# Kernel tuning notes

Hardware: AMD Instinct MI355X
Metric: run time of the kernel (lower is better)

## Reference

```python
import jax, jax.numpy as jnp
import numpy as np

C = 256
D = C // 4  # shared q/k projection dim = 64
EPS_BN = 1e-5


def _bn(x, g, b, m, v):
    # inference-style BatchNorm1d over channel dim of [B, C, N]
    inv = g / jnp.sqrt(v + EPS_BN)
    return x * inv[:, None] + (b - m * inv)[:, None]


def _sa_layer(x, xyz, qk_w, v_w, v_b, tr_w, tr_b, g, b, m, var):
    h = x + xyz                                             # [B,C,N]
    q = jnp.einsum('dc,bcn->bnd', qk_w, h)                  # [B,N,D]
    k = jnp.einsum('dc,bcn->bdn', qk_w, h)                  # [B,D,N] (shared weight)
    v = jnp.einsum('oc,bcn->bon', v_w, h) + v_b[:, None]    # [B,C,N]
    energy = jnp.einsum('bnd,bdm->bnm', q, k)               # [B,N,N]
    att = jax.nn.softmax(energy, axis=-1)
    # offset-attention L1 renorm over query dim (dim=1)
    att = att / (1e-9 + att.sum(axis=1, keepdims=True))
    x_r = jnp.einsum('bcn,bnm->bcm', v, att)                # [B,C,N]
    t = jnp.einsum('oc,bcn->bon', tr_w, x - x_r) + tr_b[:, None]
    return x + jax.nn.relu(_bn(t, g, b, m, var))


def setup_inputs() -> dict:
    key = jax.random.key(0)
    ks = jax.random.split(key, 20)
    B, N = 4, 4096
    inp = {
        'x': jax.random.normal(ks[0], (B, C, N), jnp.float32),
        'xyz': jax.random.normal(ks[1], (B, N, 3), jnp.float32),
        'pos_w': jax.random.normal(ks[2], (C, 3), jnp.float32) * 0.1,
        'pos_b': jax.random.normal(ks[3], (C,), jnp.float32) * 0.05,
        'conv1_w': jax.random.normal(ks[4], (C, C), jnp.float32) * (1.0 / np.sqrt(C)),
        'bn1_g': jax.random.uniform(ks[5], (C,), jnp.float32, 0.5, 1.5),
        'bn1_b': jax.random.normal(ks[6], (C,), jnp.float32) * 0.05,
        'bn1_m': jax.random.normal(ks[7], (C,), jnp.float32) * 0.05,
        'bn1_v': jax.random.uniform(ks[8], (C,), jnp.float32, 0.5, 1.5),
        # stacked params for 4 SA layers
        'qk_w': jax.random.normal(ks[9], (4, D, C), jnp.float32) * (1.0 / np.sqrt(C)),
        'v_w': jax.random.normal(ks[10], (4, C, C), jnp.float32) * (1.0 / np.sqrt(C)),
        'v_b': jax.random.normal(ks[11], (4, C), jnp.float32) * 0.05,
        'tr_w': jax.random.normal(ks[12], (4, C, C), jnp.float32) * (1.0 / np.sqrt(C)),
        'tr_b': jax.random.normal(ks[13], (4, C), jnp.float32) * 0.05,
        'bn_g': jax.random.uniform(ks[14], (4, C), jnp.float32, 0.5, 1.5),
        'bn_b': jax.random.normal(ks[15], (4, C), jnp.float32) * 0.05,
        'bn_m': jax.random.normal(ks[16], (4, C), jnp.float32) * 0.05,
        'bn_v': jax.random.uniform(ks[17], (4, C), jnp.float32, 0.5, 1.5),
    }
    return inp


def reference(x, xyz, pos_w, pos_b, conv1_w, bn1_g, bn1_b, bn1_m, bn1_v,
              qk_w, v_w, v_b, tr_w, tr_b, bn_g, bn_b, bn_m, bn_v):
    # xyz: [B,N,3] -> permute -> [B,3,N] -> pos conv -> [B,C,N]
    pos = jnp.einsum('oc,bnc->bon', pos_w, xyz) + pos_b[:, None]
    h = jnp.einsum('oc,bcn->bon', conv1_w, x)
    h = jax.nn.relu(_bn(h, bn1_g, bn1_b, bn1_m, bn1_v))
    outs = []
    for i in range(4):
        h = _sa_layer(h, pos, qk_w[i], v_w[i], v_b[i], tr_w[i], tr_b[i],
                      bn_g[i], bn_b[i], bn_m[i], bn_v[i])
        outs.append(h)
    return jnp.concatenate(outs, axis=1)  # [B, 4C, N]
```

## Files before the change

### kernel.cpp

```cpp
#include <hip/hip_runtime.h>

#define NB 4
#define NC 256
#define ND 64
#define NN 4096

typedef unsigned short us;
using short8v = __attribute__((ext_vector_type(8))) short;
using f32x4   = __attribute__((ext_vector_type(4))) float;

#define MFMA16 __builtin_amdgcn_mfma_f32_16x16x32_bf16

constexpr size_t SBCN = (size_t)NB * NC * NN;
constexpr size_t SBN  = (size_t)NB * NN;

__device__ inline us f2bf(float f) {
  unsigned u = __builtin_bit_cast(unsigned, f);
  u += 0x7fffu + ((u >> 16) & 1u);
  return (us)(u >> 16);
}
__device__ inline float bf2f(us s) {
  unsigned u = (unsigned)s << 16;
  return __builtin_bit_cast(float, u);
}

__global__ __launch_bounds__(256) void pos_kernel(
    const float* __restrict__ xyz, const float* __restrict__ pw,
    const float* __restrict__ pb, float* __restrict__ pos)
{
  int idx = blockIdx.x * 256 + threadIdx.x;
  int n  = idx & (NN - 1);
  int tc = idx >> 12;
  int o  = tc & (NC - 1);
  int b  = tc >> 8;
  const float* xp = xyz + ((size_t)b * NN + n) * 3;
  pos[idx] = pb[o] + pw[o*3+0]*xp[0] + pw[o*3+1]*xp[1] + pw[o*3+2]*xp[2];
}

template<int O, bool ADD_P, bool HAS_BIAS, bool HAS_BN, bool RELU,
         bool HAS_RES, bool TRIPLE, bool VSPLIT, bool HAS_OUT2>
__global__ __launch_bounds__(256) void wgemm(
    const float* __restrict__ W, const float* __restrict__ H,
    const float* __restrict__ P, const float* __restrict__ bias,
    const float* __restrict__ bng, const float* __restrict__ bnb,
    const float* __restrict__ bnm, const float* __restrict__ bnv,
    const float* __restrict__ RES, float* __restrict__ OUT,
    float* __restrict__ OUT2, float* __restrict__ OUT3,
    float* __restrict__ OUT4)
{
  __shared__ float Wt[16][64];
  __shared__ float Ht[16][64];
  const int b  = blockIdx.z;
  const int o0 = blockIdx.y * 64;
  const int n0 = blockIdx.x * 64;
  const int t  = threadIdx.x;
  const int og = t >> 4, ng = t & 15;
  const int lo = t >> 2, lc4 = (t & 3) * 4;
  const int hc = t >> 4, hn4 = (t & 15) * 4;
  float acc[4][4] = {};
  for (int c0 = 0; c0 < NC; c0 += 16) {
    float4 w4 = *(const float4*)&W[(size_t)(o0 + lo) * NC + c0 + lc4];
    float4 h4 = *(const float4*)&H[((size_t)b * NC + c0 + hc) * NN + n0 + hn4];
    if (ADD_P) {
      float4 p4 = *(const float4*)&P[((size_t)b * NC + c0 + hc) * NN + n0 + hn4];
      h4.x += p4.x; h4.y += p4.y; h4.z += p4.z; h4.w += p4.w;
    }
    Wt[lc4+0][lo] = w4.x; Wt[lc4+1][lo] = w4.y;
    Wt[lc4+2][lo] = w4.z; Wt[lc4+3][lo] = w4.w;
    *(float4*)&Ht[hc][hn4] = h4;
    __syncthreads();
    #pragma unroll
    for (int cc = 0; cc < 16; ++cc) {
      float4 wv = *(const float4*)&Wt[cc][og*4];
      float4 hv = *(const float4*)&Ht[cc][ng*4];
      float wa[4] = {wv.x, wv.y, wv.z, wv.w};
      float ha[4] = {hv.x, hv.y, hv.z, hv.w};
      #pragma unroll
      for (int i = 0; i < 4; ++i)
        #pragma unroll
        for (int j = 0; j < 4; ++j)
          acc[i][j] += wa[i] * ha[j];
    }
    __syncthreads();
  }
  float vals[4][4];
  #pragma unroll
  for (int i = 0; i < 4; ++i) {
    const int o = o0 + og * 4 + i;
    float sc = 1.0f, sh = 0.0f;
    if (HAS_BIAS) sh = bias[o];
    if (HAS_BN) {
      float inv = bng[o] * rsqrtf(bnv[o] + 1e-5f);
      sh = sh * inv + (bnb[o] - bnm[o] * inv);
      sc = inv;
    }
    #pragma unroll
    for (int j = 0; j < 4; ++j) {
      float v = acc[i][j] * sc + sh;
      if (RELU) v = fmaxf(v, 0.0f);
      vals[i][j] = v;
    }
    if (HAS_RES) {
      float4 rv = *(const float4*)&RES[((size_t)b * NC + o) * NN + n0 + ng*4];
      vals[i][0] += rv.x; vals[i][1] += rv.y;
      vals[i][2] += rv.z; vals[i][3] += rv.w;
    }
  }
  if (TRIPLE) {
    us* o1 = (us*)OUT;  us* o2 = (us*)OUT2;  us* o3 = (us*)OUT3;
    #pragma unroll
    for (int j = 0; j < 4; ++j) {
      const int n = n0 + ng * 4 + j;
      us s1[4], s2[4], s3[4];
      #pragma unroll
      for (int i = 0; i < 4; ++i) {
        float v = vals[i][j];
        us h1 = f2bf(v); float r = v - bf2f(h1);
        us h2 = f2bf(r); r -= bf2f(h2);
        us h3 = f2bf(r);
        s1[i] = h1; s2[i] = h2; s3[i] = h3;
      }
      const size_t base = ((size_t)b * NN + n) * 64 + og * 4;
      uint2 u;
      u.x = (unsigned)s1[0] | ((unsigned)s1[1] << 16);
      u.y = (unsigned)s1[2] | ((unsigned)s1[3] << 16);
      *(uint2*)&o1[base] = u;
      u.x = (unsigned)s2[0] | ((unsigned)s2[1] << 16);
      u.y = (unsigned)s2[2] | ((unsigned)s2[3] << 16);
      *(uint2*)&o2[base] = u;
      u.x = (unsigned)s3[0] | ((unsigned)s3[1] << 16);
      u.y = (unsigned)s3[2] | ((unsigned)s3[3] << 16);
      *(uint2*)&o3[base] = u;
    }
  } else if (VSPLIT) {
    us* v1p = (us*)OUT; us* v2p = (us*)OUT2;
    #pragma unroll
    for (int i = 0; i < 4; ++i) {
      const int o = o0 + og * 4 + i;
      us s1[4], s2[4];
      #pragma unroll
      for (int j = 0; j < 4; ++j) {
        float v = vals[i][j];
        us h1 = f2bf(v);
        s1[j] = h1;
        s2[j] = f2bf(v - bf2f(h1));
      }
      const size_t base = ((size_t)b * NC + o) * NN + n0 + ng * 4;
      uint2 u;
      u.x = (unsigned)s1[0] | ((unsigned)s1[1] << 16);
      u.y = (unsigned)s1[2] | ((unsigned)s1[3] << 16);
      *(uint2*)&v1p[base] = u;
      u.x = (unsigned)s2[0] | ((unsigned)s2[1] << 16);
      u.y = (unsigned)s2[2] | ((unsigned)s2[3] << 16);
      *(uint2*)&v2p[base] = u;
    }
  } else {
    #pragma unroll
    for (int i = 0; i < 4; ++i) {
      const int o = o0 + og * 4 + i;
      float4 r = {vals[i][0], vals[i][1], vals[i][2], vals[i][3]};
      *(float4*)&OUT[((size_t)b * O + o) * NN + n0 + ng*4] = r;
      if (HAS_OUT2)
        *(float4*)&OUT2[((size_t)b * 4 * NC + o) * NN + n0 + ng*4] = r;
    }
  }
}

__global__ __launch_bounds__(128, 3) void rowstats_mfma(
    const us* __restrict__ q1, const us* __restrict__ q2,
    const us* __restrict__ q3,
    float* __restrict__ Mp, float* __restrict__ Lp)
{
  __shared__ us qs[3][32][72];
  const int b = blockIdx.y;
  const int n0 = blockIdx.x * 32;
  const int mk = blockIdx.z;
  const int t = threadIdx.x;
  const int w = t >> 6, l = t & 63, lm = l & 15, g = l >> 4;
  const int nrow = n0 + w * 16;
  const us* qp[3] = {q1, q2, q3};
  short8v an[3][2];
  #pragma unroll
  for (int s = 0; s < 3; ++s) {
    const size_t ab = ((size_t)b * NN + nrow + lm) * ND + 8 * g;
    an[s][0] = *(const short8v*)(qp[s] + ab);
    an[s][1] = *(const short8v*)(qp[s] + ab + 32);
  }
  float mrun[4], lrun[4];
  #pragma unroll
  for (int r = 0; r < 4; ++r) { mrun[r] = -1e30f; lrun[r] = 0.f; }

  const int nloc0 = t >> 3, d8 = (t & 7) * 8;
  const int mbeg = mk * (NN / 2), mend = mbeg + NN / 2;
  for (int m0 = mbeg; m0 < mend; m0 += 32) {
    __syncthreads();
    #pragma unroll
    for (int i = 0; i < 6; ++i) {
      const int s = i >> 1, n = (i & 1) * 16 + nloc0;
      *(short8v*)&qs[s][n][d8] =
          *(const short8v*)(qp[s] + ((size_t)b * NN + m0 + n) * ND + d8);
    }
    __syncthreads();
    float e[2][4];
    #pragma unroll
    for (int sub = 0; sub < 2; ++sub) {
      f32x4 eA = {0.f,0.f,0.f,0.f}, eB = {0.f,0.f,0.f,0.f};
      #pragma unroll
      for (int kh = 0; kh < 2; ++kh) {
        short8v b0 = *(const short8v*)&qs[0][sub*16+lm][kh*32+8*g];
        short8v b1 = *(const short8v*)&qs[1][sub*16+lm][kh*32+8*g];
        short8v b2 = *(const short8v*)&qs[2][sub*16+lm][kh*32+8*g];
        eA = MFMA16(an[0][kh], b0, eA, 0,0,0);
        eA = MFMA16(an[0][kh], b1, eA, 0,0,0);
        eA = MFMA16(an[0][kh], b2, eA, 0,0,0);
        eB = MFMA16(an[1][kh], b0, eB, 0,0,0);
        eB = MFMA16(an[2][kh], b0, eB, 0,0,0);
        eB = MFMA16(an[1][kh], b1, eB, 0,0,0);
      }
      f32x4 ee = eA + eB;
      #pragma unroll
      for (int r = 0; r < 4; ++r) e[sub][r] = ee[r];
    }
    #pragma unroll
    for (int r = 0; r < 4; ++r) {
      float mx = fmaxf(e[0][r], e[1][r]);
      float p = __expf(e[0][r] - mx) + __expf(e[1][r] - mx);
      float d = mx - mrun[r];
      if (d > 8.f) { lrun[r] = lrun[r] * __expf(-d) + p; mrun[r] = mx; }
      else          lrun[r] += p * __expf(d);
    }
  }
  #pragma unroll
  for (int r = 0; r < 4; ++r) {
    float m = mrun[r], s = lrun[r];
    #pragma unroll
    for (int off = 1; off < 16; off <<= 1) {
      float om = __shfl_xor(m, off);
      float os = __shfl_xor(s, off);
      float nm = fmaxf(m, om);
      s = s * __expf(m - nm) + os * __expf(om - nm);
      m = nm;
    }
    if (lm == 0) {
      Mp[(size_t)mk * SBN + (size_t)b * NN + nrow + 4 * g + r] = m;
      Lp[(size_t)mk * SBN + (size_t)b * NN + nrow + 4 * g + r] = s;
    }
  }
}

__global__ __launch_bounds__(256) void statmerge(
    const float* __restrict__ Mp, const float* __restrict__ Lp,
    float* __restrict__ Mr, float* __restrict__ Lr)
{
  const int i = blockIdx.x * 256 + threadIdx.x;
  float m0 = Mp[i], m1 = Mp[SBN + i];
  float l0 = Lp[i], l1 = Lp[SBN + i];
  float M = fmaxf(m0, m1);
  float L = l0 * __expf(m0 - M) + l1 * __expf(m1 - M);
  Mr[i] = M;
  Lr[i] = 1.0f / L;
}

__global__ __launch_bounds__(256, 4) void fusedatt_mfma(
    const us* __restrict__ q1, const us* __restrict__ q2,
    const us* __restrict__ q3,
    const us* __restrict__ v1, const us* __restrict__ v2,
    const float* __restrict__ Mr, const float* __restrict__ Lr,
    float* __restrict__ xr, float* __restrict__ csb)
{
  __shared__ us qs[2][3][32][72];
  __shared__ us att1[64][40];
  __shared__ us att2[64][40];
  const int b  = blockIdx.y;
  const int m0 = blockIdx.x * 64;
  const int chalf = blockIdx.z & 1;
  const int nk    = blockIdx.z >> 1;
  const int c0 = chalf * 128;
  const int t  = threadIdx.x;
  const int w  = t >> 6, l = t & 63, lm = l & 15, g = l >> 4;
  const int mrow = w * 16 + lm;
  const int mg   = m0 + mrow;
  const us* qp[3] = {q1, q2, q3};

  short8v bm[3][2];
  #pragma unroll
  for (int s = 0; s < 3; ++s) {
    const size_t mb = ((size_t)b * NN + mg) * ND + 8 * g;
    bm[s][0] = *(const short8v*)(qp[s] + mb);
    bm[s][1] = *(const short8v*)(qp[s] + mb + 32);
  }
  const float* Mb = Mr + (size_t)b * NN;
  const float* Lb = Lr + (size_t)b * NN;
  const us* vb1 = v1 + ((size_t)b * NC + c0 + w * 32 + lm) * NN + 8 * g;
  const us* vb2 = v2 + ((size_t)b * NC + c0 + w * 32 + lm) * NN + 8 * g;

  f32x4 acc[2][4];
  const f32x4 fzero = {0.f,0.f,0.f,0.f};
  #pragma unroll
  for (int cs = 0; cs < 2; ++cs)
    #pragma unroll
    for (int mm = 0; mm < 4; ++mm) acc[cs][mm] = fzero;
  float csp = 0.f;

  const int nloc = t >> 3, d8 = (t & 7) * 8;
  const int nbeg = nk * (NN / 2), nend = nbeg + NN / 2;

  #pragma unroll
  for (int i = 0; i < 3; ++i)
    *(short8v*)&qs[0][i][nloc][d8] =
        *(const short8v*)(qp[i] + ((size_t)b * NN + nbeg + nloc) * ND + d8);
  __syncthreads();

  int cur = 0;
  for (int nt = nbeg; nt < nend; nt += 32) {
    short8v nx0, nx1, nx2;
    const bool has_next = (nt + 32) < nend;
    if (has_next) {
      const size_t nb = ((size_t)b * NN + nt + 32 + nloc) * ND + d8;
      nx0 = *(const short8v*)(qp[0] + nb);
      nx1 = *(const short8v*)(qp[1] + nb);
      nx2 = *(const short8v*)(qp[2] + nb);
    }
    #pragma unroll
    for (int sub = 0; sub < 2; ++sub) {
      f32x4 eA = fzero, eB = fzero;
      #pragma unroll
      for (int kh = 0; kh < 2; ++kh) {
        short8v a0 = *(const short8v*)&qs[cur][0][sub*16+lm][kh*32+8*g];
        short8v a1 = *(const short8v*)&qs[cur][1][sub*16+lm][kh*32+8*g];
        short8v a2 = *(const short8v*)&qs[cur][2][sub*16+lm][kh*32+8*g];
        eA = MFMA16(a0, bm[0][kh], eA, 0,0,0);
        eA = MFMA16(a0, bm[1][kh], eA, 0,0,0);
        eA = MFMA16(a0, bm[2][kh], eA, 0,0,0);
        eB = MFMA16(a1, bm[0][kh], eB, 0,0,0);
        eB = MFMA16(a2, bm[0][kh], eB, 0,0,0);
        eB = MFMA16(a1, bm[1][kh], eB, 0,0,0);
      }
      f32x4 ee = eA + eB;
      float m4[4], l4[4];
      *(float4*)m4 = *(const float4*)&Mb[nt + sub*16 + 4*g];
      *(float4*)l4 = *(const float4*)&Lb[nt + sub*16 + 4*g];
      us a1r[4], a2r[4];
      #pragma unroll
      for (int r = 0; r < 4; ++r) {
        float p = __expf(ee[r] - m4[r]) * l4[r];
        csp += p;
        us hi = f2bf(p);
        a1r[r] = hi;
        a2r[r] = f2bf(p - bf2f(hi));
      }
      uint2 u;
      u.x = (unsigned)a1r[0] | ((unsigned)a1r[1] << 16);
      u.y = (unsigned)a1r[2] | ((unsigned)a1r[3] << 16);
      *(uint2*)&att1[mrow][sub*16 + 4*g] = u;
      u.x = (unsigned)a2r[0] | ((unsigned)a2r[1] << 16);
      u.y = (unsigned)a2r[2] | ((unsigned)a2r[3] << 16);
      *(uint2*)&att2[mrow][sub*16 + 4*g] = u;
    }
    if (has_next) {
      *(short8v*)&qs[cur ^ 1][0][nloc][d8] = nx0;
      *(short8v*)&qs[cur ^ 1][1][nloc][d8] = nx1;
      *(short8v*)&qs[cur ^ 1][2][nloc][d8] = nx2;
    }
    __syncthreads();
    #pragma unroll
    for (int cs = 0; cs < 2; ++cs) {
      short8v av1 = *(const short8v*)(vb1 + (size_t)cs * 16 * NN + nt);
      short8v av2 = *(const short8v*)(vb2 + (size_t)cs * 16 * NN + nt);
      #pragma unroll
      for (int mm = 0; mm < 4; ++mm) {
        short8v batt1 = *(const short8v*)&att1[mm * 16 + lm][8 * g];
        short8v batt2 = *(const short8v*)&att2[mm * 16 + lm][8 * g];
        acc[cs][mm] = MFMA16(av1, batt1, acc[cs][mm], 0,0,0);
        acc[cs][mm] = MFMA16(av2, batt1, acc[cs][mm], 0,0,0);
        acc[cs][mm] = MFMA16(av1, batt2, acc[cs][mm], 0,0,0);
      }
    }
    __syncthreads();
    cur ^= 1;
  }

  csp += __shfl_xor(csp, 16);
  csp += __shfl_xor(csp, 32);
  if (chalf == 0 && l < 16)
    csb[(size_t)nk * SBN + (size_t)b * NN + m0 + w * 16 + l] = csp;

  float* xrp = xr + (size_t)nk * SBCN;
  #pragma unroll
  for (int cs = 0; cs < 2; ++cs) {
    #pragma unroll
    for (int mm = 0; mm < 4; ++mm) {
      #pragma unroll
      for (int r = 0; r < 4; ++r) {
        const int c = c0 + w * 32 + cs * 16 + 4 * g + r;
        const int m = m0 + mm * 16 + lm;
        xrp[((size_t)b * NC + c) * NN + m] = acc[cs][mm][r];
      }
    }
  }
}

__global__ __launch_bounds__(256) void xr_reduce(
    const float* __restrict__ xr, const float* __restrict__ csb,
    const float* __restrict__ h, float* __restrict__ dbuf)
{
  const int i4 = blockIdx.x * 256 + threadIdx.x;
  const int mq = i4 & (NN / 4 - 1);
  const int bc = i4 >> 10;
  const int b  = bc >> 8;
  const size_t off = (size_t)bc * NN + mq * 4;
  float4 a0 = *(const float4*)&xr[off];
  float4 a1 = *(const float4*)&xr[SBCN + off];
  float4 hv = *(const float4*)&h[off];
  const size_t co = (size_t)b * NN + mq * 4;
  float4 c0 = *(const float4*)&csb[co];
  float4 c1 = *(const float4*)&csb[SBN + co];
  float4 r;
  r.x = hv.x - (a0.x + a1.x) / (1e-9f + c0.x + c1.x);
  r.y = hv.y - (a0.y + a1.y) / (1e-9f + c0.y + c1.y);
  r.z = hv.z - (a0.z + a1.z) / (1e-9f + c0.z + c1.z);
  r.w = hv.w - (a0.w + a1.w) / (1e-9f + c0.w + c1.w);
  *(float4*)&dbuf[off] = r;
}

extern "C" void kernel_launch(void* const* d_in, const int* in_sizes, int n_in,
                              void* d_out, int out_size, void* d_ws, size_t ws_size,
                              hipStream_t stream) {
  const float* x      = (const float*)d_in[0];
  const float* xyz    = (const float*)d_in[1];
  const float* pos_w  = (const float*)d_in[2];
  const float* pos_b  = (const float*)d_in[3];
  const float* conv1w = (const float*)d_in[4];
  const float* bn1_g  = (const float*)d_in[5];
  const float* bn1_b  = (const float*)d_in[6];
  const float* bn1_m  = (const float*)d_in[7];
  const float* bn1_v  = (const float*)d_in[8];
  const float* qk_w   = (const float*)d_in[9];
  const float* v_w    = (const float*)d_in[10];
  const float* v_b    = (const float*)d_in[11];
  const float* tr_w   = (const float*)d_in[12];
  const float* tr_b   = (const float*)d_in[13];
  const float* bn_g   = (const float*)d_in[14];
  const float* bn_b   = (const float*)d_in[15];
  const float* bn_m   = (const float*)d_in[16];
  const float* bn_v   = (const float*)d_in[17];
  float* out = (float*)d_out;
  float* ws  = (float*)d_ws;

  const size_t BCN = SBCN;
  const size_t BDN = (size_t)NB * ND * NN;
  const size_t BN  = SBN;
  float* pos  = ws;
  float* h    = pos + BCN;
  float* xr   = h   + BCN;
  float* Mr   = xr  + 2 * BCN;
  float* Lr   = Mr  + BN;
  float* csb  = Lr  + BN;
  float* Mp   = csb + 2 * BN;
  float* Lp   = Mp  + 2 * BN;
  us* qA1 = (us*)(Lp + 2 * BN);
  us* qA2 = qA1 + BDN;
  us* qA3 = qA2 + BDN;
  us* v1  = qA3 + BDN;
  us* v2  = v1  + BCN;

  pos_kernel<<<(NB * NC * NN) / 256, 256, 0, stream>>>(xyz, pos_w, pos_b, pos);

  wgemm<256, false, false, true, true, false, false, false, false>
      <<<dim3(NN/64, NC/64, NB), 256, 0, stream>>>(
          conv1w, x, nullptr, nullptr, bn1_g, bn1_b, bn1_m, bn1_v,
          nullptr, h, nullptr, nullptr, nullptr);

  for (int li = 0; li < 4; ++li) {
    const float* qw = qk_w + (size_t)li * ND * NC;
    const float* vw = v_w  + (size_t)li * NC * NC;
    const float* vb = v_b  + (size_t)li * NC;
    const float* tw = tr_w + (size_t)li * NC * NC;
    const float* tb = tr_b + (size_t)li * NC;

    wgemm<64, true, false, false, false, false, true, false, false>
        <<<dim3(NN/64, 1, NB), 256, 0, stream>>>(
            qw, h, pos, nullptr, nullptr, nullptr, nullptr, nullptr,
            nullptr, (float*)qA1, (float*)qA2, (float*)qA3, nullptr);

    wgemm<256, true, true, false, false, false, false, true, false>
        <<<dim3(NN/64, NC/64, NB), 256, 0, stream>>>(
            vw, h, pos, vb, nullptr, nullptr, nullptr, nullptr,
            nullptr, (float*)v1, (float*)v2, nullptr, nullptr);

    rowstats_mfma<<<dim3(NN/32, NB, 2), 128, 0, stream>>>(
        qA1, qA2, qA3, Mp, Lp);
    statmerge<<<(unsigned)(BN / 256), 256, 0, stream>>>(Mp, Lp, Mr, Lr);

    fusedatt_mfma<<<dim3(NN/64, NB, 4), 256, 0, stream>>>(
        qA1, qA2, qA3, v1, v2, Mr, Lr, xr, csb);

    xr_reduce<<<(unsigned)(BCN / 1024), 256, 0, stream>>>(xr, csb, h, xr);

    wgemm<256, false, true, true, true, true, false, false, true>
        <<<dim3(NN/64, NC/64, NB), 256, 0, stream>>>(
            tw, xr, nullptr, tb, bn_g + li*NC, bn_b + li*NC,
            bn_m + li*NC, bn_v + li*NC,
            h, h, out + (size_t)li * NC * NN, nullptr, nullptr);
  }
}
```

Measured before the change: 1.605 ms.

## Enlarge wgemm output tile and make attention blocks cover all channels

The fp32 weight GEMMs now use a 128-row output tile, so each thread holds 8x4 accumulators and each loaded H tile is reused across twice as many output channels. The fused attention kernel drops the channel-half split: each block computes all 256 channels, so the softmax attention tile (exp recomputation from q) is built once instead of twice. Register pressure rises and occupancy falls (launch bounds go from 4 to 2 blocks), and the attention grid halves, which may reduce latency hiding.

Result: no change. 1.614 ms (+0.6%).

```diff
diff --git a/kernel.cpp b/kernel.cpp
--- a/kernel.cpp
+++ b/kernel.cpp
@@ -37,7 +37,7 @@
   pos[idx] = pb[o] + pw[o*3+0]*xp[0] + pw[o*3+1]*xp[1] + pw[o*3+2]*xp[2];
 }
 
-template<int O, bool ADD_P, bool HAS_BIAS, bool HAS_BN, bool RELU,
+template<int OTILE, int O, bool ADD_P, bool HAS_BIAS, bool HAS_BN, bool RELU,
          bool HAS_RES, bool TRIPLE, bool VSPLIT, bool HAS_OUT2>
 __global__ __launch_bounds__(256) void wgemm(
     const float* __restrict__ W, const float* __restrict__ H,
@@ -48,45 +48,60 @@
     float* __restrict__ OUT2, float* __restrict__ OUT3,
     float* __restrict__ OUT4)
 {
-  __shared__ float Wt[16][64];
+  constexpr int R = OTILE / 16;
+  __shared__ float Wt[16][OTILE + 4];
   __shared__ float Ht[16][64];
   const int b  = blockIdx.z;
-  const int o0 = blockIdx.y * 64;
+  const int o0 = blockIdx.y * OTILE;
   const int n0 = blockIdx.x * 64;
   const int t  = threadIdx.x;
   const int og = t >> 4, ng = t & 15;
-  const int lo = t >> 2, lc4 = (t & 3) * 4;
   const int hc = t >> 4, hn4 = (t & 15) * 4;
-  float acc[4][4] = {};
+  float acc[R][4] = {};
   for (int c0 = 0; c0 < NC; c0 += 16) {
-    float4 w4 = *(const float4*)&W[(size_t)(o0 + lo) * NC + c0 + lc4];
+    if constexpr (OTILE == 64) {
+      const int lo = t >> 2, lc4 = (t & 3) * 4;
+      float4 w4 = *(const float4*)&W[(size_t)(o0 + lo) * NC + c0 + lc4];
+      Wt[lc4+0][lo] = w4.x; Wt[lc4+1][lo] = w4.y;
+      Wt[lc4+2][lo] = w4.z; Wt[lc4+3][lo] = w4.w;
+    } else {
+      const int lo = t >> 1, lc8 = (t & 1) * 8;
+      const float* wp = &W[(size_t)(o0 + lo) * NC + c0 + lc8];
+      float4 wa = *(const float4*)wp;
+      float4 wb = *(const float4*)(wp + 4);
+      Wt[lc8+0][lo] = wa.x; Wt[lc8+1][lo] = wa.y;
+      Wt[lc8+2][lo] = wa.z; Wt[lc8+3][lo] = wa.w;
+      Wt[lc8+4][lo] = wb.x; Wt[lc8+5][lo] = wb.y;
+      Wt[lc8+6][lo] = wb.z; Wt[lc8+7][lo] = wb.w;
+    }
     float4 h4 = *(const float4*)&H[((size_t)b * NC + c0 + hc) * NN + n0 + hn4];
     if (ADD_P) {
       float4 p4 = *(const float4*)&P[((size_t)b * NC + c0 + hc) * NN + n0 + hn4];
       h4.x += p4.x; h4.y += p4.y; h4.z += p4.z; h4.w += p4.w;
     }
-    Wt[lc4+0][lo] = w4.x; Wt[lc4+1][lo] = w4.y;
-    Wt[lc4+2][lo] = w4.z; Wt[lc4+3][lo] = w4.w;
     *(float4*)&Ht[hc][hn4] = h4;
     __syncthreads();
     #pragma unroll
     for (int cc = 0; cc < 16; ++cc) {
-      float4 wv = *(const float4*)&Wt[cc][og*4];
       float4 hv = *(const float4*)&Ht[cc][ng*4];
-      float wa[4] = {wv.x, wv.y, wv.z, wv.w};
       float ha[4] = {hv.x, hv.y, hv.z, hv.w};
       #pragma unroll
-      for (int i = 0; i < 4; ++i)
+      for (int rq = 0; rq < R / 4; ++rq) {
+        float4 wv = *(const float4*)&Wt[cc][og * R + rq * 4];
+        float wa[4] = {wv.x, wv.y, wv.z, wv.w};
         #pragma unroll
-        for (int j = 0; j < 4; ++j)
-          acc[i][j] += wa[i] * ha[j];
+        for (int i = 0; i < 4; ++i)
+          #pragma unroll
+          for (int j = 0; j < 4; ++j)
+            acc[rq * 4 + i][j] += wa[i] * ha[j];
+      }
     }
     __syncthreads();
   }
-  float vals[4][4];
-  #pragma unroll
-  for (int i = 0; i < 4; ++i) {
-    const int o = o0 + og * 4 + i;
+  float vals[R][4];
+  #pragma unroll
+  for (int i = 0; i < R; ++i) {
+    const int o = o0 + og * R + i;
     float sc = 1.0f, sh = 0.0f;
     if (HAS_BIAS) sh = bias[o];
     if (HAS_BN) {
@@ -111,16 +126,16 @@
     #pragma unroll
     for (int j = 0; j < 4; ++j) {
       const int n = n0 + ng * 4 + j;
-      us s1[4], s2[4], s3[4];
-      #pragma unroll
-      for (int i = 0; i < 4; ++i) {
+      us s1[R], s2[R], s3[R];
+      #pragma unroll
+      for (int i = 0; i < R; ++i) {
         float v = vals[i][j];
         us h1 = f2bf(v); float r = v - bf2f(h1);
         us h2 = f2bf(r); r -= bf2f(h2);
         us h3 = f2bf(r);
         s1[i] = h1; s2[i] = h2; s3[i] = h3;
       }
-      const size_t base = ((size_t)b * NN + n) * 64 + og * 4;
+      const size_t base = ((size_t)b * NN + n) * 64 + og * R;
       uint2 u;
       u.x = (unsigned)s1[0] | ((unsigned)s1[1] << 16);
       u.y = (unsigned)s1[2] | ((unsigned)s1[3] << 16);
@@ -135,8 +150,8 @@
   } else if (VSPLIT) {
     us* v1p = (us*)OUT; us* v2p = (us*)OUT2;
     #pragma unroll
-    for (int i = 0; i < 4; ++i) {
-      const int o = o0 + og * 4 + i;
+    for (int i = 0; i < R; ++i) {
+      const int o = o0 + og * R + i;
       us s1[4], s2[4];
       #pragma unroll
       for (int j = 0; j < 4; ++j) {
@@ -156,8 +171,8 @@
     }
   } else {
     #pragma unroll
-    for (int i = 0; i < 4; ++i) {
-      const int o = o0 + og * 4 + i;
+    for (int i = 0; i < R; ++i) {
+      const int o = o0 + og * R + i;
       float4 r = {vals[i][0], vals[i][1], vals[i][2], vals[i][3]};
       *(float4*)&OUT[((size_t)b * O + o) * NN + n0 + ng*4] = r;
       if (HAS_OUT2)
@@ -261,7 +276,7 @@
   Lr[i] = 1.0f / L;
 }
 
-__global__ __launch_bounds__(256, 4) void fusedatt_mfma(
+__global__ __launch_bounds__(256, 2) void fusedatt_mfma(
     const us* __restrict__ q1, const us* __restrict__ q2,
     const us* __restrict__ q3,
     const us* __restrict__ v1, const us* __restrict__ v2,
@@ -273,9 +288,7 @@
   __shared__ us att2[64][40];
   const int b  = blockIdx.y;
   const int m0 = blockIdx.x * 64;
-  const int chalf = blockIdx.z & 1;
-  const int nk    = blockIdx.z >> 1;
-  const int c0 = chalf * 128;
+  const int nk = blockIdx.z;
   const int t  = threadIdx.x;
   const int w  = t >> 6, l = t & 63, lm = l & 15, g = l >> 4;
   const int mrow = w * 16 + lm;
@@ -291,13 +304,13 @@
   }
   const float* Mb = Mr + (size_t)b * NN;
   const float* Lb = Lr + (size_t)b * NN;
-  const us* vb1 = v1 + ((size_t)b * NC + c0 + w * 32 + lm) * NN + 8 * g;
-  const us* vb2 = v2 + ((size_t)b * NC + c0 + w * 32 + lm) * NN + 8 * g;
-
-  f32x4 acc[2][4];
+  const us* vb1 = v1 + ((size_t)b * NC + w * 64 + lm) * NN + 8 * g;
+  const us* vb2 = v2 + ((size_t)b * NC + w * 64 + lm) * NN + 8 * g;
+
+  f32x4 acc[4][4];
   const f32x4 fzero = {0.f,0.f,0.f,0.f};
   #pragma unroll
-  for (int cs = 0; cs < 2; ++cs)
+  for (int cs = 0; cs < 4; ++cs)
     #pragma unroll
     for (int mm = 0; mm < 4; ++mm) acc[cs][mm] = fzero;
   float csp = 0.f;
@@ -364,7 +377,7 @@
     }
     __syncthreads();
     #pragma unroll
-    for (int cs = 0; cs < 2; ++cs) {
+    for (int cs = 0; cs < 4; ++cs) {
       short8v av1 = *(const short8v*)(vb1 + (size_t)cs * 16 * NN + nt);
       short8v av2 = *(const short8v*)(vb2 + (size_t)cs * 16 * NN + nt);
       #pragma unroll
@@ -382,17 +395,17 @@
 
   csp += __shfl_xor(csp, 16);
   csp += __shfl_xor(csp, 32);
-  if (chalf == 0 && l < 16)
+  if (l < 16)
     csb[(size_t)nk * SBN + (size_t)b * NN + m0 + w * 16 + l] = csp;
 
   float* xrp = xr + (size_t)nk * SBCN;
   #pragma unroll
-  for (int cs = 0; cs < 2; ++cs) {
+  for (int cs = 0; cs < 4; ++cs) {
     #pragma unroll
     for (int mm = 0; mm < 4; ++mm) {
       #pragma unroll
       for (int r = 0; r < 4; ++r) {
-        const int c = c0 + w * 32 + cs * 16 + 4 * g + r;
+        const int c = w * 64 + cs * 16 + 4 * g + r;
         const int m = m0 + mm * 16 + lm;
         xrp[((size_t)b * NC + c) * NN + m] = acc[cs][mm][r];
       }
@@ -466,8 +479,8 @@
 
   pos_kernel<<<(NB * NC * NN) / 256, 256, 0, stream>>>(xyz, pos_w, pos_b, pos);
 
-  wgemm<256, false, false, true, true, false, false, false, false>
-      <<<dim3(NN/64, NC/64, NB), 256, 0, stream>>>(
+  wgemm<128, 256, false, false, true, true, false, false, false, false>
+      <<<dim3(NN/64, NC/128, NB), 256, 0, stream>>>(
           conv1w, x, nullptr, nullptr, bn1_g, bn1_b, bn1_m, bn1_v,
           nullptr, h, nullptr, nullptr, nullptr);
 
@@ -478,13 +491,13 @@
     const float* tw = tr_w + (size_t)li * NC * NC;
     const float* tb = tr_b + (size_t)li * NC;
 
-    wgemm<64, true, false, false, false, false, true, false, false>
+    wgemm<64, 64, true, false, false, false, false, true, false, false>
         <<<dim3(NN/64, 1, NB), 256, 0, stream>>>(
             qw, h, pos, nullptr, nullptr, nullptr, nullptr, nullptr,
             nullptr, (float*)qA1, (float*)qA2, (float*)qA3, nullptr);
 
-    wgemm<256, true, true, false, false, false, false, true, false>
-        <<<dim3(NN/64, NC/64, NB), 256, 0, stream>>>(
+    wgemm<128, 256, true, true, false, false, false, false, true, false>
+        <<<dim3(NN/64, NC/128, NB), 256, 0, stream>>>(
             vw, h, pos, vb, nullptr, nullptr, nullptr, nullptr,
             nullptr, (float*)v1, (float*)v2, nullptr, nullptr);
 
@@ -492,13 +505,13 @@
         qA1, qA2, qA3, Mp, Lp);
     statmerge<<<(unsigned)(BN / 256), 256, 0, stream>>>(Mp, Lp, Mr, Lr);
 
-    fusedatt_mfma<<<dim3(NN/64, NB, 4), 256, 0, stream>>>(
+    fusedatt_mfma<<<dim3(NN/64, NB, 2), 256, 0, stream>>>(
         qA1, qA2, qA3, v1, v2, Mr, Lr, xr, csb);
 
     xr_reduce<<<(unsigned)(BCN / 1024), 256, 0, stream>>>(xr, csb, h, xr);
 
-    wgemm<256, false, true, true, true, true, false, false, true>
-        <<<dim3(NN/64, NC/64, NB), 256, 0, stream>>>(
+    wgemm<128, 256, false, true, true, true, true, false, false, true>
+        <<<dim3(NN/64, NC/128, NB), 256, 0, stream>>>(
             tw, xr, nullptr, tb, bn_g + li*NC, bn_b + li*NC,
             bn_m + li*NC, bn_v + li*NC,
             h, h, out + (size_t)li * NC * NN, nullptr, nullptr);
```
